# Optimization experiments

Measured on AMD Instinct MI355X. Metric: run time of the kernel, lower is better.

Reference implementation:

```python
import jax, jax.numpy as jnp
import numpy as np
from jax import lax

E4M3 = jnp.float8_e4m3fn
DIM_NUMS = (((1,), (0,)), ((), ()))  # contract inputs last dim with kernel first dim


def quantize_dequantize(x, q_dtype, scale, compute_dtype):
    dtype_max = jnp.finfo(q_dtype).max.astype(compute_dtype)
    s = scale.astype(compute_dtype)
    scaled = x.astype(compute_dtype) / s
    clipped = jnp.clip(scaled, -dtype_max, dtype_max)
    qx = clipped.astype(q_dtype)
    # dequantize back to x.dtype
    return qx.astype(x.dtype) * scale.astype(x.dtype)


def setup_inputs() -> dict:
    key = jax.random.key(0)
    k1, k2 = jax.random.split(key)
    H = 1024  # amax_history_length
    return {
        "inputs": jax.random.normal(k1, (8192, 4096), dtype=jnp.float32),
        "kernel": jax.random.normal(k2, (4096, 4096), dtype=jnp.float32),
        "input_scale": jnp.ones((1,), jnp.float32),
        "input_amax_history": jnp.zeros((H,), jnp.float32),
        "kernel_scale": jnp.ones((1,), jnp.float32),
        "kernel_amax_history": jnp.zeros((H,), jnp.float32),
        "output_grad_scale": jnp.ones((1,), jnp.float32),
        "output_grad_amax_history": jnp.zeros((H,), jnp.float32),
    }


def reference(inputs, kernel, input_scale, input_amax_history, kernel_scale,
              kernel_amax_history, output_grad_scale, output_grad_amax_history):
    comp_dtype = kernel.dtype
    inputs = jnp.asarray(inputs, comp_dtype)
    # in_qdq on both operands (e4m3); out_qdq is identity in the forward pass.
    lhs_qdq = quantize_dequantize(inputs, E4M3, input_scale, comp_dtype)
    rhs_qdq = quantize_dequantize(kernel, E4M3, kernel_scale, comp_dtype)
    out = lax.dot_general(lhs_qdq, rhs_qdq, DIM_NUMS, precision=None)
    return out
```

## Files before the change

kernel.cpp:

```cpp
#include <hip/hip_runtime.h>
#include <stdint.h>

#define M_DIM 8192
#define N_DIM 4096
#define K_DIM 4096
#define NT (K_DIM / 128)

typedef float f32x4 __attribute__((ext_vector_type(4)));
typedef int v4i __attribute__((ext_vector_type(4)));
typedef int v8i __attribute__((ext_vector_type(8)));
typedef uint32_t u32;


__device__ __forceinline__ void gload_lds16(const void* g, void* l) {
  __builtin_amdgcn_global_load_lds(
      (__attribute__((address_space(1))) void*)(g),
      (__attribute__((address_space(3))) void*)(l), 16, 0, 0);
}

__device__ __forceinline__ float clipdiv(float v, float s) {
  v = v / s;
  return fminf(fmaxf(v, -448.f), 448.f);
}

__device__ __forceinline__ u32 pack4_fp8(float a, float b, float c, float d) {
  int w = __builtin_amdgcn_cvt_pk_fp8_f32(a, b, 0, false);
  w = __builtin_amdgcn_cvt_pk_fp8_f32(c, d, w, true);
  return (u32)w;
}


__global__ __launch_bounds__(256) void quant_a(const float* __restrict__ x,
                                               u32* __restrict__ q,
                                               const float* __restrict__ scale,
                                               int nv4) {
  int base = blockIdx.x * 1024 + threadIdx.x;
  float s = scale[0];
#pragma unroll
  for (int r = 0; r < 4; ++r) {
    int idx = base + r * 256;
    if (idx < nv4) {
      float4 v = ((const float4*)x)[idx];
      q[idx] = pack4_fp8(clipdiv(v.x, s), clipdiv(v.y, s),
                         clipdiv(v.z, s), clipdiv(v.w, s));
    }
  }
}


__global__ __launch_bounds__(256) void quant_b_t(const float* __restrict__ B,
                                                 uint8_t* __restrict__ qT,
                                                 const float* __restrict__ scale) {
  __shared__ __align__(16) uint8_t lt[64 * 80];
  int tid = threadIdx.x;
  int kt = blockIdx.x * 64;
  int nt = blockIdx.y * 64;
  float s = scale[0];

  int kl = tid >> 4;
  int n4 = (tid & 15) * 4;
#pragma unroll
  for (int rep = 0; rep < 4; ++rep) {
    int k = kl + rep * 16;
    float4 v = *(const float4*)&B[(long)(kt + k) * N_DIM + nt + n4];
    u32 w = pack4_fp8(clipdiv(v.x, s), clipdiv(v.y, s),
                      clipdiv(v.z, s), clipdiv(v.w, s));
    lt[(n4 + 0) * 80 + k] = (uint8_t)(w & 0xff);
    lt[(n4 + 1) * 80 + k] = (uint8_t)((w >> 8) & 0xff);
    lt[(n4 + 2) * 80 + k] = (uint8_t)((w >> 16) & 0xff);
    lt[(n4 + 3) * 80 + k] = (uint8_t)(w >> 24);
  }
  __syncthreads();
  int n = tid >> 2, ch = tid & 3;
  uint4 o = *(const uint4*)&lt[n * 80 + ch * 16];
  *(uint4*)&qT[(long)(nt + n) * K_DIM + kt + ch * 16] = o;
}


template <int Q, int MQ, int NQ, int BUF, int SMAT, int SH, int SBUF, int VM>
__device__ __forceinline__ void phase(uint8_t* lds, const int (&offA)[4][2],
                                      const int (&offB)[2][2],
                                      f32x4 (&acc)[4][4][2], int st,
                                      const uint8_t* pA0, const uint8_t* pA1,
                                      const uint8_t* pB0, const uint8_t* pB1,
                                      int ld0, int ld1) {
  const uint8_t* Ab = lds + BUF * 32768 + MQ * 16384;
  const uint8_t* Bb = lds + 65536 + BUF * 32768 + NQ * 16384;
  v8i a[4], b[2];
#pragma unroll
  for (int mi = 0; mi < 4; ++mi) {
    v4i lo = *(const v4i*)(Ab + offA[mi][0]);
    v4i hi = *(const v4i*)(Ab + offA[mi][1]);
    a[mi] = __builtin_shufflevector(lo, hi, 0, 1, 2, 3, 4, 5, 6, 7);
  }
#pragma unroll
  for (int nj = 0; nj < 2; ++nj) {
    v4i lo = *(const v4i*)(Bb + offB[nj][0]);
    v4i hi = *(const v4i*)(Bb + offB[nj][1]);
    b[nj] = __builtin_shufflevector(lo, hi, 0, 1, 2, 3, 4, 5, 6, 7);
  }
  {
    long ko = (long)((st & (NT - 1)) * 128) + (long)SH * (128L * (long)K_DIM);
    const uint8_t* s0 = (SMAT ? pB0 : pA0) + ko;
    const uint8_t* s1 = (SMAT ? pB1 : pA1) + ko;
    uint8_t* d0 = lds + SMAT * 65536 + SBUF * 32768 + SH * 16384 + ld0;
    uint8_t* d1 = lds + SMAT * 65536 + SBUF * 32768 + SH * 16384 + ld1;
    gload_lds16(s0, d0);
    gload_lds16(s1, d1);
  }
  asm volatile("s_waitcnt lgkmcnt(8)" ::: "memory");
  __builtin_amdgcn_s_barrier();
  asm volatile("s_waitcnt lgkmcnt(0)" ::: "memory");
  __builtin_amdgcn_sched_barrier(0);
  __builtin_amdgcn_s_setprio(1);
#pragma unroll
  for (int mi = 0; mi < 4; ++mi)
#pragma unroll
    for (int nj = 0; nj < 2; ++nj)
      acc[Q][mi][nj] = __builtin_amdgcn_mfma_scale_f32_16x16x128_f8f6f4(
          a[mi], b[nj], acc[Q][mi][nj], 0, 0, 0, 0x7f7f7f7f, 0, 0x7f7f7f7f);
  __builtin_amdgcn_s_setprio(0);
  if (VM) asm volatile("s_waitcnt vmcnt(4)" ::: "memory");
  __builtin_amdgcn_s_barrier();
}

__global__ __launch_bounds__(512, 2) void gemm_mx8(const uint8_t* __restrict__ Aq,
                                                   const uint8_t* __restrict__ BqT,
                                                   float* __restrict__ C,
                                                   const float* __restrict__ sA,
                                                   const float* __restrict__ sB) {
  __shared__ __align__(16) uint8_t lds[131072];

  const int tid = threadIdx.x;
  const int lane = tid & 63;
  const int wid = tid >> 6;
  const int wr = wid >> 2;
  const int wc = wid & 3;
  const int r16 = lane & 15;
  const int hi = lane >> 4;

  int bid = blockIdx.x;
  int wg = (bid & 7) * 64 + (bid >> 3);
  const long bm = (long)(wg >> 4) * 256;
  const long bn = (long)(wg & 15) * 256;

  float s = sA[0] * sB[0];
  asm volatile("" ::"v"(s));

  const int gid0 = tid, gid1 = tid + 512;
  const int row0 = gid0 >> 3, row1 = gid1 >> 3;
  const int sc0 = ((gid0 & 7) ^ (row0 & 7)) << 4;
  const int sc1 = ((gid1 & 7) ^ (row1 & 7)) << 4;
  const uint8_t* pA0 = Aq + (bm + row0) * (long)K_DIM + sc0;
  const uint8_t* pA1 = Aq + (bm + row1) * (long)K_DIM + sc1;
  const uint8_t* pB0 = BqT + (bn + row0) * (long)K_DIM + sc0;
  const uint8_t* pB1 = BqT + (bn + row1) * (long)K_DIM + sc1;
  const int ld0 = gid0 * 16, ld1 = gid1 * 16;

#define STG(MAT, H, T, BUF)                                                   \
  do {                                                                        \
    long ko = (long)(((T) & (NT - 1)) * 128) + (long)(H) * (128L * K_DIM);    \
    gload_lds16((MAT ? pB0 : pA0) + ko,                                       \
                lds + (MAT)*65536 + (BUF)*32768 + (H)*16384 + ld0);           \
    gload_lds16((MAT ? pB1 : pA1) + ko,                                       \
                lds + (MAT)*65536 + (BUF)*32768 + (H)*16384 + ld1);           \
  } while (0)

  int offA[4][2], offB[2][2];
#pragma unroll
  for (int mi = 0; mi < 4; ++mi) {
    int ra = wr * 64 + mi * 16 + r16;
#pragma unroll
    for (int g = 0; g < 2; ++g) {
      int lg = 2 * hi + g;
      offA[mi][g] = ra * 128 + ((lg ^ (ra & 7)) << 4);
    }
  }
#pragma unroll
  for (int nj = 0; nj < 2; ++nj) {
    int rb = wc * 32 + nj * 16 + r16;
#pragma unroll
    for (int g = 0; g < 2; ++g) {
      int lg = 2 * hi + g;
      offB[nj][g] = rb * 128 + ((lg ^ (rb & 7)) << 4);
    }
  }

  f32x4 acc[4][4][2] = {};

  STG(0, 0, 0, 0);
  STG(0, 1, 0, 0);
  STG(1, 0, 0, 0);
  STG(1, 1, 0, 0);
  STG(0, 0, 1, 1);
  STG(1, 1, 1, 1);
  asm volatile("s_waitcnt vmcnt(4)" ::: "memory");
  __builtin_amdgcn_s_barrier();

  for (int i = 0; i < NT / 2; ++i) {
    int T = 2 * i;
    phase<0, 0, 0, 0, 0, 1, 1, 0>(lds, offA, offB, acc, T + 1, pA0, pA1, pB0, pB1, ld0, ld1);
    phase<1, 0, 1, 0, 1, 0, 1, 0>(lds, offA, offB, acc, T + 1, pA0, pA1, pB0, pB1, ld0, ld1);
    phase<3, 1, 1, 0, 0, 0, 0, 0>(lds, offA, offB, acc, T + 2, pA0, pA1, pB0, pB1, ld0, ld1);
    phase<2, 1, 0, 0, 1, 1, 0, 1>(lds, offA, offB, acc, T + 2, pA0, pA1, pB0, pB1, ld0, ld1);
    phase<0, 0, 0, 1, 0, 1, 0, 0>(lds, offA, offB, acc, T + 2, pA0, pA1, pB0, pB1, ld0, ld1);
    phase<1, 0, 1, 1, 1, 0, 0, 0>(lds, offA, offB, acc, T + 2, pA0, pA1, pB0, pB1, ld0, ld1);
    phase<3, 1, 1, 1, 0, 0, 1, 0>(lds, offA, offB, acc, T + 3, pA0, pA1, pB0, pB1, ld0, ld1);
    phase<2, 1, 0, 1, 1, 1, 1, 1>(lds, offA, offB, acc, T + 3, pA0, pA1, pB0, pB1, ld0, ld1);
  }
#undef STG

#pragma unroll
  for (int MQ = 0; MQ < 2; ++MQ)
#pragma unroll
    for (int NQ = 0; NQ < 2; ++NQ)
#pragma unroll
      for (int mi = 0; mi < 4; ++mi)
#pragma unroll
        for (int nj = 0; nj < 2; ++nj) {
          long row = bm + MQ * 128 + wr * 64 + mi * 16 + hi * 4;
          long col = bn + NQ * 128 + wc * 32 + nj * 16 + r16;
          float* cp = C + row * N_DIM + col;
          f32x4 v = acc[MQ * 2 + NQ][mi][nj];
#pragma unroll
          for (int e = 0; e < 4; ++e) cp[(long)e * N_DIM] = v[e] * s;
        }
}


extern "C" void kernel_launch(void* const* d_in, const int* in_sizes, int n_in,
                              void* d_out, int out_size, void* d_ws, size_t ws_size,
                              hipStream_t stream) {
  const float* A = (const float*)d_in[0];
  const float* B = (const float*)d_in[1];
  const float* sA = (const float*)d_in[2];
  const float* sB = (const float*)d_in[4];
  float* out = (float*)d_out;

  uint8_t* Aq = (uint8_t*)d_ws;
  uint8_t* BqT = Aq + (size_t)M_DIM * K_DIM;

  int nv4_a = M_DIM * K_DIM / 4;
  quant_a<<<nv4_a / 1024, 256, 0, stream>>>(A, (u32*)Aq, sA, nv4_a);
  quant_b_t<<<dim3(K_DIM / 64, N_DIM / 64), 256, 0, stream>>>(B, BqT, sB);
  gemm_mx8<<<dim3((M_DIM / 256) * (N_DIM / 256)), 512, 0, stream>>>(Aq, BqT, out, sA, sB);
}
```

Before: 225.2 us.

## Remap warp tiles to 128x64 per wave with B fragments reused across A rows

Changes the per-wave output mapping from four scattered 64x32 quadrant tiles to one contiguous 128x64 tile. Each k-tile now loads four B fragments once and reuses them across eight A fragments, reducing LDS reads per MFMA. The load/compute schedule is reorganized into per-k-tile groups of four sub-phases with the same global-to-LDS staging. Risks are higher register pressure and the removal of the lgkmcnt(8) partial wait before the barrier. The prologue also changes one staged load from A half 0 to B half 0 at tile 1, which alters the prefetch order.

```diff
diff --git a/kernel.cpp b/kernel.cpp
--- a/kernel.cpp
+++ b/kernel.cpp
@@ -27,6 +27,17 @@
   int w = __builtin_amdgcn_cvt_pk_fp8_f32(a, b, 0, false);
   w = __builtin_amdgcn_cvt_pk_fp8_f32(c, d, w, true);
   return (u32)w;
+}
+
+__device__ __forceinline__ v8i rd8(const void* lo, const void* hi) {
+  v4i l = *(const v4i*)lo;
+  v4i h = *(const v4i*)hi;
+  return __builtin_shufflevector(l, h, 0, 1, 2, 3, 4, 5, 6, 7);
+}
+
+__device__ __forceinline__ f32x4 mfma8(v8i a, v8i b, f32x4 c) {
+  return __builtin_amdgcn_mfma_scale_f32_16x16x128_f8f6f4(
+      a, b, c, 0, 0, 0, 0x7f7f7f7f, 0, 0x7f7f7f7f);
 }
 
 
@@ -77,51 +88,56 @@
 }
 
 
-template <int Q, int MQ, int NQ, int BUF, int SMAT, int SH, int SBUF, int VM>
-__device__ __forceinline__ void phase(uint8_t* lds, const int (&offA)[4][2],
-                                      const int (&offB)[2][2],
-                                      f32x4 (&acc)[4][4][2], int st,
-                                      const uint8_t* pA0, const uint8_t* pA1,
+__device__ __forceinline__ void stg(uint8_t* lds, const uint8_t* pA0,
+                                    const uint8_t* pA1, const uint8_t* pB0,
+                                    const uint8_t* pB1, int ld0, int ld1,
+                                    int mat, int h, int t, int buf) {
+  long ko = (long)((t & (NT - 1)) * 128) + (long)h * (128L * (long)K_DIM);
+  const uint8_t* s0 = (mat ? pB0 : pA0) + ko;
+  const uint8_t* s1 = (mat ? pB1 : pA1) + ko;
+  uint8_t* d0 = lds + mat * 65536 + buf * 32768 + h * 16384 + ld0;
+  uint8_t* d1 = lds + mat * 65536 + buf * 32768 + h * 16384 + ld1;
+  gload_lds16(s0, d0);
+  gload_lds16(s1, d1);
+}
+
+template <int BUF, int SEL>
+__device__ __forceinline__ void ktile(uint8_t* lds, const int (&offA)[8][2],
+                                      const int (&offB)[4][2], f32x4 (&acc)[8][4],
+                                      int T, const uint8_t* pA0, const uint8_t* pA1,
                                       const uint8_t* pB0, const uint8_t* pB1,
-                                      int ld0, int ld1) {
-  const uint8_t* Ab = lds + BUF * 32768 + MQ * 16384;
-  const uint8_t* Bb = lds + 65536 + BUF * 32768 + NQ * 16384;
-  v8i a[4], b[2];
-#pragma unroll
-  for (int mi = 0; mi < 4; ++mi) {
-    v4i lo = *(const v4i*)(Ab + offA[mi][0]);
-    v4i hi = *(const v4i*)(Ab + offA[mi][1]);
-    a[mi] = __builtin_shufflevector(lo, hi, 0, 1, 2, 3, 4, 5, 6, 7);
-  }
-#pragma unroll
-  for (int nj = 0; nj < 2; ++nj) {
-    v4i lo = *(const v4i*)(Bb + offB[nj][0]);
-    v4i hi = *(const v4i*)(Bb + offB[nj][1]);
-    b[nj] = __builtin_shufflevector(lo, hi, 0, 1, 2, 3, 4, 5, 6, 7);
-  }
-  {
-    long ko = (long)((st & (NT - 1)) * 128) + (long)SH * (128L * (long)K_DIM);
-    const uint8_t* s0 = (SMAT ? pB0 : pA0) + ko;
-    const uint8_t* s1 = (SMAT ? pB1 : pA1) + ko;
-    uint8_t* d0 = lds + SMAT * 65536 + SBUF * 32768 + SH * 16384 + ld0;
-    uint8_t* d1 = lds + SMAT * 65536 + SBUF * 32768 + SH * 16384 + ld1;
-    gload_lds16(s0, d0);
-    gload_lds16(s1, d1);
-  }
-  asm volatile("s_waitcnt lgkmcnt(8)" ::: "memory");
-  __builtin_amdgcn_s_barrier();
-  asm volatile("s_waitcnt lgkmcnt(0)" ::: "memory");
-  __builtin_amdgcn_sched_barrier(0);
-  __builtin_amdgcn_s_setprio(1);
-#pragma unroll
-  for (int mi = 0; mi < 4; ++mi)
-#pragma unroll
-    for (int nj = 0; nj < 2; ++nj)
-      acc[Q][mi][nj] = __builtin_amdgcn_mfma_scale_f32_16x16x128_f8f6f4(
-          a[mi], b[nj], acc[Q][mi][nj], 0, 0, 0, 0x7f7f7f7f, 0, 0x7f7f7f7f);
-  __builtin_amdgcn_s_setprio(0);
-  if (VM) asm volatile("s_waitcnt vmcnt(4)" ::: "memory");
-  __builtin_amdgcn_s_barrier();
+                                      int ld0, int ld1, int abase, int bbase) {
+  constexpr int SM_[2][4] = {{0, 0, 1, 1}, {0, 0, 1, 1}};
+  constexpr int SH_[2][4] = {{0, 1, 0, 1}, {0, 1, 0, 1}};
+  constexpr int DT_[2][4] = {{1, 1, 2, 2}, {2, 2, 3, 3}};
+  constexpr int SB_[2][4] = {{1, 1, 0, 0}, {0, 0, 1, 1}};
+
+  const uint8_t* Ab = lds + BUF * 32768 + abase;
+  const uint8_t* Bb = lds + 65536 + BUF * 32768 + bbase;
+
+  v8i b[4];
+#pragma unroll
+  for (int nj = 0; nj < 4; ++nj) b[nj] = rd8(Bb + offB[nj][0], Bb + offB[nj][1]);
+
+#pragma unroll
+  for (int p = 0; p < 4; ++p) {
+    v8i a0 = rd8(Ab + offA[2 * p][0], Ab + offA[2 * p][1]);
+    v8i a1 = rd8(Ab + offA[2 * p + 1][0], Ab + offA[2 * p + 1][1]);
+    stg(lds, pA0, pA1, pB0, pB1, ld0, ld1, SM_[SEL][p], SH_[SEL][p],
+        T + DT_[SEL][p], SB_[SEL][p]);
+    __builtin_amdgcn_s_barrier();
+    asm volatile("s_waitcnt lgkmcnt(0)" ::: "memory");
+    __builtin_amdgcn_sched_barrier(0);
+    __builtin_amdgcn_s_setprio(1);
+#pragma unroll
+    for (int nj = 0; nj < 4; ++nj) {
+      acc[2 * p][nj] = mfma8(a0, b[nj], acc[2 * p][nj]);
+      acc[2 * p + 1][nj] = mfma8(a1, b[nj], acc[2 * p + 1][nj]);
+    }
+    __builtin_amdgcn_s_setprio(0);
+    if (p == 3) asm volatile("s_waitcnt vmcnt(4)" ::: "memory");
+    __builtin_amdgcn_s_barrier();
+  }
 }
 
 __global__ __launch_bounds__(512, 2) void gemm_mx8(const uint8_t* __restrict__ Aq,
@@ -156,20 +172,13 @@
   const uint8_t* pB0 = BqT + (bn + row0) * (long)K_DIM + sc0;
   const uint8_t* pB1 = BqT + (bn + row1) * (long)K_DIM + sc1;
   const int ld0 = gid0 * 16, ld1 = gid1 * 16;
-
-#define STG(MAT, H, T, BUF)                                                   \
-  do {                                                                        \
-    long ko = (long)(((T) & (NT - 1)) * 128) + (long)(H) * (128L * K_DIM);    \
-    gload_lds16((MAT ? pB0 : pA0) + ko,                                       \
-                lds + (MAT)*65536 + (BUF)*32768 + (H)*16384 + ld0);           \
-    gload_lds16((MAT ? pB1 : pA1) + ko,                                       \
-                lds + (MAT)*65536 + (BUF)*32768 + (H)*16384 + ld1);           \
-  } while (0)
-
-  int offA[4][2], offB[2][2];
-#pragma unroll
-  for (int mi = 0; mi < 4; ++mi) {
-    int ra = wr * 64 + mi * 16 + r16;
+  const int abase = wr * 16384;
+  const int bbase = (wc >> 1) * 16384;
+
+  int offA[8][2], offB[4][2];
+#pragma unroll
+  for (int mi = 0; mi < 8; ++mi) {
+    int ra = mi * 16 + r16;
 #pragma unroll
     for (int g = 0; g < 2; ++g) {
       int lg = 2 * hi + g;
@@ -177,8 +186,8 @@
     }
   }
 #pragma unroll
-  for (int nj = 0; nj < 2; ++nj) {
-    int rb = wc * 32 + nj * 16 + r16;
+  for (int nj = 0; nj < 4; ++nj) {
+    int rb = (wc & 1) * 64 + nj * 16 + r16;
 #pragma unroll
     for (int g = 0; g < 2; ++g) {
       int lg = 2 * hi + g;
@@ -186,45 +195,34 @@
     }
   }
 
-  f32x4 acc[4][4][2] = {};
-
-  STG(0, 0, 0, 0);
-  STG(0, 1, 0, 0);
-  STG(1, 0, 0, 0);
-  STG(1, 1, 0, 0);
-  STG(0, 0, 1, 1);
-  STG(1, 1, 1, 1);
+  f32x4 acc[8][4] = {};
+
+  stg(lds, pA0, pA1, pB0, pB1, ld0, ld1, 0, 0, 0, 0);
+  stg(lds, pA0, pA1, pB0, pB1, ld0, ld1, 0, 1, 0, 0);
+  stg(lds, pA0, pA1, pB0, pB1, ld0, ld1, 1, 0, 0, 0);
+  stg(lds, pA0, pA1, pB0, pB1, ld0, ld1, 1, 1, 0, 0);
+  stg(lds, pA0, pA1, pB0, pB1, ld0, ld1, 1, 0, 1, 1);
+  stg(lds, pA0, pA1, pB0, pB1, ld0, ld1, 1, 1, 1, 1);
   asm volatile("s_waitcnt vmcnt(4)" ::: "memory");
   __builtin_amdgcn_s_barrier();
 
   for (int i = 0; i < NT / 2; ++i) {
     int T = 2 * i;
-    phase<0, 0, 0, 0, 0, 1, 1, 0>(lds, offA, offB, acc, T + 1, pA0, pA1, pB0, pB1, ld0, ld1);
-    phase<1, 0, 1, 0, 1, 0, 1, 0>(lds, offA, offB, acc, T + 1, pA0, pA1, pB0, pB1, ld0, ld1);
-    phase<3, 1, 1, 0, 0, 0, 0, 0>(lds, offA, offB, acc, T + 2, pA0, pA1, pB0, pB1, ld0, ld1);
-    phase<2, 1, 0, 0, 1, 1, 0, 1>(lds, offA, offB, acc, T + 2, pA0, pA1, pB0, pB1, ld0, ld1);
-    phase<0, 0, 0, 1, 0, 1, 0, 0>(lds, offA, offB, acc, T + 2, pA0, pA1, pB0, pB1, ld0, ld1);
-    phase<1, 0, 1, 1, 1, 0, 0, 0>(lds, offA, offB, acc, T + 2, pA0, pA1, pB0, pB1, ld0, ld1);
-    phase<3, 1, 1, 1, 0, 0, 1, 0>(lds, offA, offB, acc, T + 3, pA0, pA1, pB0, pB1, ld0, ld1);
-    phase<2, 1, 0, 1, 1, 1, 1, 1>(lds, offA, offB, acc, T + 3, pA0, pA1, pB0, pB1, ld0, ld1);
-  }
-#undef STG
-
-#pragma unroll
-  for (int MQ = 0; MQ < 2; ++MQ)
-#pragma unroll
-    for (int NQ = 0; NQ < 2; ++NQ)
-#pragma unroll
-      for (int mi = 0; mi < 4; ++mi)
-#pragma unroll
-        for (int nj = 0; nj < 2; ++nj) {
-          long row = bm + MQ * 128 + wr * 64 + mi * 16 + hi * 4;
-          long col = bn + NQ * 128 + wc * 32 + nj * 16 + r16;
-          float* cp = C + row * N_DIM + col;
-          f32x4 v = acc[MQ * 2 + NQ][mi][nj];
-#pragma unroll
-          for (int e = 0; e < 4; ++e) cp[(long)e * N_DIM] = v[e] * s;
-        }
+    ktile<0, 0>(lds, offA, offB, acc, T, pA0, pA1, pB0, pB1, ld0, ld1, abase, bbase);
+    ktile<1, 1>(lds, offA, offB, acc, T, pA0, pA1, pB0, pB1, ld0, ld1, abase, bbase);
+  }
+
+#pragma unroll
+  for (int mi = 0; mi < 8; ++mi)
+#pragma unroll
+    for (int nj = 0; nj < 4; ++nj) {
+      long row = bm + wr * 128 + mi * 16 + hi * 4;
+      long col = bn + wc * 64 + nj * 16 + r16;
+      float* cp = C + row * N_DIM + col;
+      f32x4 v = acc[mi][nj];
+#pragma unroll
+      for (int e = 0; e < 4; ++e) cp[(long)e * N_DIM] = v[e] * s;
+    }
 }
 
 
```

Result: slower. 300.7 us (+33.5%).
